# Optimization experiments

Hardware: AMD Instinct MI355X
Metric: run time of the kernel (lower is better)

Reference implementation:

```python
import jax, jax.numpy as jnp
import numpy as np

N_NODES = 100000
N_EDGES = 3200000
STATE_DIM = 128
ACTION_DIM = 8


def _w(key, shape, scale=0.05):
    return (jax.random.normal(key, shape, dtype=jnp.float32) * scale)


def setup_inputs() -> dict:
    key = jax.random.key(0)
    ks = jax.random.split(key, 24)
    x = jax.random.normal(ks[0], (N_NODES, STATE_DIM), dtype=jnp.float32)
    edge_index = jax.random.randint(ks[1], (2, N_EDGES), 0, N_NODES, dtype=jnp.int64)
    inp = {
        "x": x,
        "edge_index": edge_index,
        # GCN layers (weights stored [in, out] so forward is x @ W + b)
        "W1": _w(ks[2], (STATE_DIM, 128)), "b1": jnp.zeros((128,), jnp.float32),
        "W2": _w(ks[3], (128, 128)),       "b2": jnp.zeros((128,), jnp.float32),
        "W3": _w(ks[4], (128, 64)),        "b3": jnp.zeros((64,), jnp.float32),
        # actor MLP 64->128->64->ACTION_DIM + softmax
        "Wa1": _w(ks[5], (64, 128)),  "ba1": jnp.zeros((128,), jnp.float32),
        "Wa2": _w(ks[6], (128, 64)),  "ba2": jnp.zeros((64,), jnp.float32),
        "Wa3": _w(ks[7], (64, ACTION_DIM)), "ba3": jnp.zeros((ACTION_DIM,), jnp.float32),
        # critic MLP 64->128->64->1
        "Wc1": _w(ks[8], (64, 128)),  "bc1": jnp.zeros((128,), jnp.float32),
        "Wc2": _w(ks[9], (128, 64)),  "bc2": jnp.zeros((64,), jnp.float32),
        "Wc3": _w(ks[10], (64, 1)),   "bc3": jnp.zeros((1,), jnp.float32),
    }
    return inp


def _gcn_conv(x, W, b, src, dst, norm):
    # GCNConv: D^{-1/2} (A + I) D^{-1/2} X W + b  (self loops already in src/dst)
    h = x @ W                                   # [N, out]
    msg = h[src] * norm[:, None]                # gather + per-edge scale
    agg = jax.ops.segment_sum(msg, dst, num_segments=N_NODES)
    return agg + b


def reference(x, edge_index,
              W1, b1, W2, b2, W3, b3,
              Wa1, ba1, Wa2, ba2, Wa3, ba3,
              Wc1, bc1, Wc2, bc2, Wc3, bc3):
    loop = jnp.arange(N_NODES, dtype=edge_index.dtype)
    src = jnp.concatenate([edge_index[0], loop])
    dst = jnp.concatenate([edge_index[1], loop])
    deg = jax.ops.segment_sum(jnp.ones_like(dst, dtype=x.dtype), dst,
                              num_segments=N_NODES)
    dinv = jax.lax.rsqrt(deg)                   # deg >= 1 via self loops
    norm = dinv[src] * dinv[dst]                # [E+N]

    # forward_gnn (dropout is identity in eval mode)
    h = jax.nn.relu(_gcn_conv(x, W1, b1, src, dst, norm))
    h = jax.nn.relu(_gcn_conv(h, W2, b2, src, dst, norm))
    h = _gcn_conv(h, W3, b3, src, dst, norm)    # [N, 64]

    a = jax.nn.relu(h @ Wa1 + ba1)
    a = jax.nn.relu(a @ Wa2 + ba2)
    probs = jax.nn.softmax(a @ Wa3 + ba3, axis=-1)   # [N, ACTION_DIM]

    c = jax.nn.relu(h @ Wc1 + bc1)
    c = jax.nn.relu(c @ Wc2 + bc2)
    values = c @ Wc3 + bc3                      # [N, 1]

    return jnp.concatenate([probs, values], axis=-1)  # [N, ACTION_DIM+1]
```

## Files before the change

kernel.cpp:

```cpp
#include <hip/hip_runtime.h>
#include <hip/hip_bf16.h>
#include <math.h>


#define WS_ALIGN(x) (((x) + 255) & ~(size_t)255)

constexpr int RNG  = 64;
constexpr int NRG  = 1563;
constexpr int NB   = 1024;
constexpr int CHK  = 16;

constexpr float S_FP8     = 64.0f;
constexpr float S_FP8_INV = 1.0f / 64.0f;

using bf16x8 = __attribute__((ext_vector_type(8))) short;
using f32x4  = __attribute__((ext_vector_type(4))) float;
using f32x2  = __attribute__((ext_vector_type(2))) float;

__device__ __forceinline__ float b2f(unsigned short u) {
    return __uint_as_float(((unsigned int)u) << 16);
}
__device__ __forceinline__ unsigned short f2b(float f) {
    __hip_bfloat16 hb = __float2bfloat16(f);
    return *(unsigned short*)&hb;
}
__device__ __forceinline__ unsigned char f2fp8(float f) {
    return (unsigned char)(__builtin_amdgcn_cvt_pk_fp8_f32(f, f, 0, false) & 0xff);
}
__device__ __forceinline__ int pad8(int v) { return (v + 7) & ~7; }

__device__ __forceinline__ void acc8(uint2 u, f32x2& a01, f32x2& a23,
                                     f32x2& a45, f32x2& a67) {
    a01 += __builtin_amdgcn_cvt_pk_f32_fp8((int)u.x, false);
    a23 += __builtin_amdgcn_cvt_pk_f32_fp8((int)u.x, true);
    a45 += __builtin_amdgcn_cvt_pk_f32_fp8((int)u.y, false);
    a67 += __builtin_amdgcn_cvt_pk_f32_fp8((int)u.y, true);
}


__global__ __launch_bounds__(256) void bucket_count_k(
    const int* __restrict__ dst, int* __restrict__ bcnt, int E) {
    __shared__ int c64[RNG];
    int b = blockIdx.x, t = threadIdx.x;
    if (t < RNG) c64[t] = 0;
    __syncthreads();
    int ec = (E + NB - 1) / NB;
    int e0 = b * ec, e1 = min(E, e0 + ec);
    for (int e = e0 + t; e < e1; e += 256) {
        int d = __builtin_nontemporal_load(dst + e);
        atomicAdd(&c64[d / NRG], 1);
    }
    __syncthreads();
    if (t < RNG) bcnt[t * NB + b] = c64[t];
}

__global__ __launch_bounds__(256) void rsum_k(
    const int* __restrict__ bcnt, int* __restrict__ base, int* __restrict__ rtot) {
    __shared__ int s[256];
    int r = blockIdx.x, t = threadIdx.x;
    const int* row = bcnt + (size_t)r * NB;
    int v[4], loc = 0;
#pragma unroll
    for (int j = 0; j < 4; j++) { v[j] = row[t * 4 + j]; loc += v[j]; }
    s[t] = loc;
    __syncthreads();
    for (int d = 1; d < 256; d <<= 1) {
        int x = (t >= d) ? s[t - d] : 0;
        __syncthreads();
        s[t] += x;
        __syncthreads();
    }
    int run = s[t] - loc;
    int* bp = base + (size_t)r * NB + t * 4;
#pragma unroll
    for (int j = 0; j < 4; j++) { bp[j] = run; run += v[j]; }
    if (t == 255) rtot[r] = s[255];
}

__global__ void rstart_k(const int* __restrict__ rtot, int* __restrict__ bstart, int E) {
    if (threadIdx.x == 0) {
        int run = 0;
        for (int r = 0; r < RNG; r++) { bstart[r] = run; run += rtot[r]; }
        bstart[RNG] = run;
    }
}

__global__ __launch_bounds__(256) void bucket_scatter_k(
    const int* __restrict__ src, const int* __restrict__ dst,
    const int* __restrict__ base, const int* __restrict__ bstart,
    unsigned* __restrict__ bucket, int E) {
    __shared__ int cur[RNG];
    int b = blockIdx.x, t = threadIdx.x;
    if (t < RNG) cur[t] = bstart[t] + base[(size_t)t * NB + b];
    __syncthreads();
    int ec = (E + NB - 1) / NB;
    int e0 = b * ec, e1 = min(E, e0 + ec);
    for (int e = e0 + t; e < e1; e += 256) {
        int d = __builtin_nontemporal_load(dst + e);
        int sv = __builtin_nontemporal_load(src + e);
        int r = d / NRG;
        int pos = atomicAdd(&cur[r], 1);
        bucket[pos] = ((unsigned)(d - r * NRG) << 17) | (unsigned)sv;
    }
}

__global__ __launch_bounds__(256) void hist_bucket_k(
    const unsigned* __restrict__ bucket, const int* __restrict__ bstart,
    int* __restrict__ hist) {
    __shared__ int h[NRG];
    int b = blockIdx.x, r = b & 63, c2 = b >> 6, t = threadIdx.x;
    for (int i = t; i < NRG; i += 256) h[i] = 0;
    int s0 = bstart[r], s1 = bstart[r + 1];
    int ec = (s1 - s0 + CHK - 1) / CHK;
    int e0 = s0 + c2 * ec, e1 = min(s1, e0 + ec);
    __syncthreads();
    for (int e = e0 + t; e < e1; e += 256) {
        unsigned v = __builtin_nontemporal_load(bucket + e);
        atomicAdd(&h[v >> 17], 1);
    }
    __syncthreads();
    int* out = hist + ((size_t)r * CHK + c2) * NRG;
    for (int i = t; i < NRG; i += 256) out[i] = h[i];
}

__global__ void sum_hist_dinv_k(const int* __restrict__ hist, int* __restrict__ cnt,
                                float* __restrict__ dinv, int N) {
    int i = blockIdx.x * 256 + threadIdx.x;
    if (i >= N) return;
    int r = i / NRG, li = i - r * NRG;
    const int* hp = hist + ((size_t)r * CHK) * NRG + li;
    int s = 0;
#pragma unroll
    for (int c = 0; c < CHK; c++) s += hp[(size_t)c * NRG];
    cnt[i] = s;
    dinv[i] = rsqrtf((float)s + 1.0f);
}

__global__ void chunk_sum_k(const int* __restrict__ cnt, int* __restrict__ bsum, int n) {
    __shared__ int sd[256];
    int t = threadIdx.x;
    int i = blockIdx.x * 256 + t;
    sd[t] = (i < n) ? pad8(cnt[i]) : 0;
    __syncthreads();
    for (int d = 128; d > 0; d >>= 1) {
        if (t < d) sd[t] += sd[t + d];
        __syncthreads();
    }
    if (t == 0) bsum[blockIdx.x] = sd[0];
}

__global__ void scan_mid_k(const int* __restrict__ bsum, int* __restrict__ boff,
                           int nb, int* __restrict__ rowptr, int N) {
    __shared__ int s[512];
    int t = threadIdx.x;
    s[t] = (t < nb) ? bsum[t] : 0;
    __syncthreads();
    if (t == 0) {
        int run = 0;
        for (int i = 0; i < nb; i++) { int v = s[i]; s[i] = run; run += v; }
        rowptr[N] = run;
    }
    __syncthreads();
    if (t < nb) boff[t] = s[t];
}

__global__ void scan_off_pad_k(const int* __restrict__ cnt, const int* __restrict__ boff,
                               int* __restrict__ rowptr, int* __restrict__ hist,
                               int* __restrict__ col, int N) {
    __shared__ int s[256];
    int t = threadIdx.x;
    int i = blockIdx.x * 256 + t;
    int cv = (i < N) ? cnt[i] : 0;
    int v = pad8(cv);
    if (i >= N) v = 0;
    s[t] = v;
    __syncthreads();
    for (int d = 1; d < 256; d <<= 1) {
        int x = (t >= d) ? s[t - d] : 0;
        __syncthreads();
        s[t] += x;
        __syncthreads();
    }
    if (i < N) {
        int rp = s[t] - v + boff[blockIdx.x];
        rowptr[i] = rp;
        int r = i / NRG, li = i - r * NRG;
        int* hp = hist + ((size_t)r * CHK) * NRG + li;
        int run = rp;
#pragma unroll
        for (int c = 0; c < CHK; c++) {
            int hv = hp[(size_t)c * NRG];
            hp[(size_t)c * NRG] = run;
            run += hv;
        }
        for (int e = rp + cv; e < rp + v; e++) col[e] = N;
    }
}

__global__ __launch_bounds__(256) void fill2_k(
    const unsigned* __restrict__ bucket, const int* __restrict__ bstart,
    const int* __restrict__ hist, int* __restrict__ col) {
    __shared__ int cur[NRG];
    int b = blockIdx.x, r = b & 63, c2 = b >> 6, t = threadIdx.x;
    const int* hp = hist + ((size_t)r * CHK + c2) * NRG;
    for (int i = t; i < NRG; i += 256) cur[i] = hp[i];
    int s0 = bstart[r], s1 = bstart[r + 1];
    int ec = (s1 - s0 + CHK - 1) / CHK;
    int e0 = s0 + c2 * ec, e1 = min(s1, e0 + ec);
    __syncthreads();
    for (int e = e0 + t; e < e1; e += 256) {
        unsigned v = __builtin_nontemporal_load(bucket + e);
        int slot = atomicAdd(&cur[v >> 17], 1);
        col[slot] = (int)(v & 0x1FFFFu);
    }
}


__global__ __launch_bounds__(256) void prep_w_k(
    const float* __restrict__ W1, const float* __restrict__ W2,
    const float* __restrict__ W3, const float* __restrict__ Wa1,
    const float* __restrict__ Wc1, const float* __restrict__ Wa2,
    const float* __restrict__ Wc2, unsigned short* __restrict__ wt) {
    int i = blockIdx.x * 256 + threadIdx.x;
    const float* W; int off, K, OUT;
    if (i < 16384)      { W = W1;  off = 0;     K = 128; OUT = 128; }
    else if (i < 32768) { W = W2;  off = 16384; K = 128; OUT = 128; }
    else if (i < 40960) { W = W3;  off = 32768; K = 128; OUT = 64; }
    else if (i < 49152) { W = Wa1; off = 40960; K = 64;  OUT = 128; }
    else if (i < 57344) { W = Wc1; off = 49152; K = 64;  OUT = 128; }
    else if (i < 65536) { W = Wa2; off = 57344; K = 128; OUT = 64; }
    else                { W = Wc2; off = 65536; K = 128; OUT = 64; }
    int j = i - off, k = j / OUT, n = j - k * OUT;
    wt[off + n * K + k] = f2b(W[j]);
}


template <int K, int OUT, int EPI, bool AF32>
__global__ __launch_bounds__(256) void gemm2_k(
    const void* __restrict__ Xv, int ldx, const unsigned short* __restrict__ Wt,
    const float* __restrict__ sb, const float* __restrict__ w3b,
    const float* __restrict__ b3, void* __restrict__ Yv, int N, int NT) {
    constexpr int LDK = K + 8;
    __shared__ __align__(16) unsigned short Bs[OUT * LDK];
    __shared__ __align__(16) unsigned short As[64 * LDK];
    int t = threadIdx.x;

    for (int g = t; g < OUT * (K / 8); g += 256) {
        int r = g / (K / 8), q = g - r * (K / 8);
        *(uint4*)&Bs[r * LDK + q * 8] = *(const uint4*)(Wt + r * K + q * 8);
    }

    int wv = t >> 6, lane = t & 63;
    int lm = lane & 15, lq = lane >> 4;
    constexpr int CT = OUT / 16;

    for (int tile = blockIdx.x; tile < NT; tile += gridDim.x) {
        int rowBase = tile * 64;

        if constexpr (AF32) {
            const float* X = (const float*)Xv;
            for (int g = t; g < 64 * (K / 8); g += 256) {
                int r = g / (K / 8), q = g - r * (K / 8);
                int gr = rowBase + r;
                unsigned short us[8];
                if (gr < N) {
                    float4 v0 = *(const float4*)(X + (size_t)gr * ldx + q * 8);
                    float4 v1 = *(const float4*)(X + (size_t)gr * ldx + q * 8 + 4);
                    us[0] = f2b(v0.x); us[1] = f2b(v0.y); us[2] = f2b(v0.z); us[3] = f2b(v0.w);
                    us[4] = f2b(v1.x); us[5] = f2b(v1.y); us[6] = f2b(v1.z); us[7] = f2b(v1.w);
                } else {
#pragma unroll
                    for (int j = 0; j < 8; j++) us[j] = 0;
                }
                *(uint4*)&As[r * LDK + q * 8] = *(uint4*)us;
            }
        } else {
            const unsigned short* X = (const unsigned short*)Xv;
            for (int g = t; g < 64 * (K / 8); g += 256) {
                int r = g / (K / 8), q = g - r * (K / 8);
                int gr = rowBase + r;
                uint4 v = make_uint4(0, 0, 0, 0);
                if (gr < N) v = *(const uint4*)(X + (size_t)gr * ldx + q * 8);
                *(uint4*)&As[r * LDK + q * 8] = v;
            }
        }
        __syncthreads();

        f32x4 acc[CT];
#pragma unroll
        for (int c = 0; c < CT; c++) acc[c] = (f32x4){0.f, 0.f, 0.f, 0.f};

        const unsigned short* arow = &As[(wv * 16 + lm) * LDK + lq * 8];
#pragma unroll
        for (int kt = 0; kt < K / 32; kt++) {
            bf16x8 a = *(const bf16x8*)(arow + kt * 32);
#pragma unroll
            for (int c = 0; c < CT; c++) {
                bf16x8 b = *(const bf16x8*)&Bs[(c * 16 + lm) * LDK + kt * 32 + lq * 8];
                acc[c] = __builtin_amdgcn_mfma_f32_16x16x32_bf16(a, b, acc[c], 0, 0, 0);
            }
        }

        int r0 = rowBase + wv * 16 + lq * 4;
        if constexpr (EPI == 0) {
#pragma unroll
            for (int r = 0; r < 4; r++) {
                int gr = r0 + r;
                float scale = (gr < N) ? sb[gr] * S_FP8 : 0.f;
#pragma unroll
                for (int c = 0; c < CT; c++) {
                    int colg = c * 16 + lm;
                    ((unsigned char*)Yv)[(size_t)gr * OUT + colg] = f2fp8(acc[c][r] * scale);
                }
            }
        } else if constexpr (EPI == 1) {
#pragma unroll
            for (int r = 0; r < 4; r++) {
                int gr = r0 + r;
                if (gr < N) {
#pragma unroll
                    for (int c = 0; c < CT; c++) {
                        int colg = c * 16 + lm;
                        float bb = (colg < 128) ? sb[colg] : w3b[colg - 128];
                        float v = fmaxf(acc[c][r] + bb, 0.f);
                        ((unsigned short*)Yv)[(size_t)gr * OUT + colg] = f2b(v);
                    }
                }
            }
        } else if constexpr (EPI == 2) {
            float l[4][8];
#pragma unroll
            for (int r = 0; r < 4; r++)
#pragma unroll
                for (int a = 0; a < 8; a++) l[r][a] = 0.f;
#pragma unroll
            for (int c = 0; c < CT; c++) {
                int colg = c * 16 + lm;
#pragma unroll
                for (int r = 0; r < 4; r++) {
                    float v = fmaxf(acc[c][r] + sb[colg], 0.f);
#pragma unroll
                    for (int a = 0; a < 8; a++)
                        l[r][a] = fmaf(v, w3b[colg * 8 + a], l[r][a]);
                }
            }
#pragma unroll
            for (int w = 1; w < 16; w <<= 1)
#pragma unroll
                for (int r = 0; r < 4; r++)
#pragma unroll
                    for (int a = 0; a < 8; a++)
                        l[r][a] += __shfl_xor(l[r][a], w, 64);
            if (lm < 8) {
#pragma unroll
                for (int r = 0; r < 4; r++) {
                    int gr = r0 + r;
                    if (gr < N) {
                        float lg[8], m = -1e30f;
#pragma unroll
                        for (int a = 0; a < 8; a++) { lg[a] = l[r][a] + b3[a]; m = fmaxf(m, lg[a]); }
                        float sum = 0.f;
#pragma unroll
                        for (int a = 0; a < 8; a++) { lg[a] = expf(lg[a] - m); sum += lg[a]; }
                        ((float*)Yv)[(size_t)gr * 9 + lm] = lg[lm] / sum;
                    }
                }
            }
        } else {
            float lv[4] = {0.f, 0.f, 0.f, 0.f};
#pragma unroll
            for (int c = 0; c < CT; c++) {
                int colg = c * 16 + lm;
#pragma unroll
                for (int r = 0; r < 4; r++) {
                    float v = fmaxf(acc[c][r] + sb[colg], 0.f);
                    lv[r] = fmaf(v, w3b[colg], lv[r]);
                }
            }
#pragma unroll
            for (int w = 1; w < 16; w <<= 1)
#pragma unroll
                for (int r = 0; r < 4; r++) lv[r] += __shfl_xor(lv[r], w, 64);
            if (lm == 0) {
#pragma unroll
                for (int r = 0; r < 4; r++) {
                    int gr = r0 + r;
                    if (gr < N) ((float*)Yv)[(size_t)gr * 9 + 8] = lv[r] + b3[0];
                }
            }
        }
        __syncthreads();
    }
}


template <bool RELU>
__global__ __launch_bounds__(256) void agg128_k(
    const unsigned char* __restrict__ H,
    const int* __restrict__ rowptr, const int* __restrict__ col,
    const float* __restrict__ dinv, const float* __restrict__ bias,
    unsigned short* __restrict__ Y, int N, int Ecap) {
    int tid = threadIdx.x;
    int node = blockIdx.x * 4 + (tid >> 6);
    if (node >= N) return;
    int lane = tid & 63;
    int grp = lane >> 4;
    int li8 = (lane & 15) * 8;

    f32x2 a01 = {0.f, 0.f}, a23 = {0.f, 0.f}, a45 = {0.f, 0.f}, a67 = {0.f, 0.f};
    if (grp == 0) {
        uint2 u = *(const uint2*)(H + (size_t)node * 128 + li8);
        acc8(u, a01, a23, a45, a67);
    }

    int start = rowptr[node], end = rowptr[node + 1];
    for (int e0 = start; e0 < end; e0 += 64) {
        int cv = col[min(e0 + lane, Ecap - 1)];
        int quads = min(64, end - e0) >> 2;
        for (int q = 0; q < quads; q += 2) {
            int s0 = __shfl(cv, 4 * q + grp, 64);
            int s1 = __shfl(cv, 4 * q + 4 + grp, 64);
            uint2 u0 = *(const uint2*)(H + (size_t)s0 * 128 + li8);
            uint2 u1 = *(const uint2*)(H + (size_t)s1 * 128 + li8);
            acc8(u0, a01, a23, a45, a67);
            acc8(u1, a01, a23, a45, a67);
        }
    }

#pragma unroll
    for (int w = 16; w < 64; w <<= 1) {
        a01[0] += __shfl_xor(a01[0], w, 64); a01[1] += __shfl_xor(a01[1], w, 64);
        a23[0] += __shfl_xor(a23[0], w, 64); a23[1] += __shfl_xor(a23[1], w, 64);
        a45[0] += __shfl_xor(a45[0], w, 64); a45[1] += __shfl_xor(a45[1], w, 64);
        a67[0] += __shfl_xor(a67[0], w, 64); a67[1] += __shfl_xor(a67[1], w, 64);
    }

    if (grp == 0) {
        float dv = dinv[node] * S_FP8_INV;
        float4 b0 = *(const float4*)(bias + li8);
        float4 b1 = *(const float4*)(bias + li8 + 4);
        float o0 = a01[0] * dv + b0.x, o1 = a01[1] * dv + b0.y;
        float o2 = a23[0] * dv + b0.z, o3 = a23[1] * dv + b0.w;
        float o4 = a45[0] * dv + b1.x, o5 = a45[1] * dv + b1.y;
        float o6 = a67[0] * dv + b1.z, o7 = a67[1] * dv + b1.w;
        if (RELU) {
            o0 = fmaxf(o0, 0.f); o1 = fmaxf(o1, 0.f); o2 = fmaxf(o2, 0.f); o3 = fmaxf(o3, 0.f);
            o4 = fmaxf(o4, 0.f); o5 = fmaxf(o5, 0.f); o6 = fmaxf(o6, 0.f); o7 = fmaxf(o7, 0.f);
        }
        unsigned short us[8] = {f2b(o0), f2b(o1), f2b(o2), f2b(o3),
                                f2b(o4), f2b(o5), f2b(o6), f2b(o7)};
        *(uint4*)(Y + (size_t)node * 128 + li8) = *(uint4*)us;
    }
}

__global__ __launch_bounds__(256) void agg64_k(
    const unsigned char* __restrict__ H,
    const int* __restrict__ rowptr, const int* __restrict__ col,
    const float* __restrict__ dinv, const float* __restrict__ bias,
    unsigned short* __restrict__ Y, int N, int Ecap) {
    int tid = threadIdx.x;
    int node = blockIdx.x * 4 + (tid >> 6);
    if (node >= N) return;
    int lane = tid & 63;
    int grp = lane >> 3;
    int li8 = (lane & 7) * 8;

    f32x2 a01 = {0.f, 0.f}, a23 = {0.f, 0.f}, a45 = {0.f, 0.f}, a67 = {0.f, 0.f};
    if (grp == 0) {
        uint2 u = *(const uint2*)(H + (size_t)node * 64 + li8);
        acc8(u, a01, a23, a45, a67);
    }

    int start = rowptr[node], end = rowptr[node + 1];
    for (int e0 = start; e0 < end; e0 += 64) {
        int cv = col[min(e0 + lane, Ecap - 1)];
        int octs = min(64, end - e0) >> 3;
        int o = 0;
        for (; o + 2 <= octs; o += 2) {
            int s0 = __shfl(cv, 8 * o + grp, 64);
            int s1 = __shfl(cv, 8 * o + 8 + grp, 64);
            uint2 u0 = *(const uint2*)(H + (size_t)s0 * 64 + li8);
            uint2 u1 = *(const uint2*)(H + (size_t)s1 * 64 + li8);
            acc8(u0, a01, a23, a45, a67);
            acc8(u1, a01, a23, a45, a67);
        }
        if (o < octs) {
            int s0 = __shfl(cv, 8 * o + grp, 64);
            uint2 u0 = *(const uint2*)(H + (size_t)s0 * 64 + li8);
            acc8(u0, a01, a23, a45, a67);
        }
    }

#pragma unroll
    for (int w = 8; w < 64; w <<= 1) {
        a01[0] += __shfl_xor(a01[0], w, 64); a01[1] += __shfl_xor(a01[1], w, 64);
        a23[0] += __shfl_xor(a23[0], w, 64); a23[1] += __shfl_xor(a23[1], w, 64);
        a45[0] += __shfl_xor(a45[0], w, 64); a45[1] += __shfl_xor(a45[1], w, 64);
        a67[0] += __shfl_xor(a67[0], w, 64); a67[1] += __shfl_xor(a67[1], w, 64);
    }

    if (grp == 0) {
        float dv = dinv[node] * S_FP8_INV;
        float4 b0 = *(const float4*)(bias + li8);
        float4 b1 = *(const float4*)(bias + li8 + 4);
        unsigned short us[8] = {
            f2b(a01[0] * dv + b0.x), f2b(a01[1] * dv + b0.y),
            f2b(a23[0] * dv + b0.z), f2b(a23[1] * dv + b0.w),
            f2b(a45[0] * dv + b1.x), f2b(a45[1] * dv + b1.y),
            f2b(a67[0] * dv + b1.z), f2b(a67[1] * dv + b1.w)};
        *(uint4*)(Y + (size_t)node * 64 + li8) = *(uint4*)us;
    }
}


extern "C" void kernel_launch(void* const* d_in, const int* in_sizes, int n_in,
                              void* d_out, int out_size, void* d_ws, size_t ws_size,
                              hipStream_t stream) {
    const float* x   = (const float*)d_in[0];
    const int*   ei  = (const int*)d_in[1];
    const float* W1  = (const float*)d_in[2];  const float* b1  = (const float*)d_in[3];
    const float* W2  = (const float*)d_in[4];  const float* b2  = (const float*)d_in[5];
    const float* W3  = (const float*)d_in[6];  const float* b3  = (const float*)d_in[7];
    const float* Wa1 = (const float*)d_in[8];  const float* ba1 = (const float*)d_in[9];
    const float* Wa2 = (const float*)d_in[10]; const float* ba2 = (const float*)d_in[11];
    const float* Wa3 = (const float*)d_in[12]; const float* ba3 = (const float*)d_in[13];
    const float* Wc1 = (const float*)d_in[14]; const float* bc1 = (const float*)d_in[15];
    const float* Wc2 = (const float*)d_in[16]; const float* bc2 = (const float*)d_in[17];
    const float* Wc3 = (const float*)d_in[18]; const float* bc3 = (const float*)d_in[19];
    float* out = (float*)d_out;

    const int N = in_sizes[0] / 128;
    const int E = in_sizes[1] / 2;
    const int* src = ei;
    const int* dst = ei + E;
    const int Ecap = E + 8 * N;
    const int Npad = ((N + 63) / 64) * 64;
    const int NT   = (N + 63) / 64;

    size_t off = 0;
    auto take = [&](size_t bytes) { size_t o = off; off = WS_ALIGN(off + bytes); return o; };
    char* ws = (char*)d_ws;
    unsigned short* h3     = (unsigned short*)(ws + take((size_t)N * 64 * 2));
    unsigned short* h      = (unsigned short*)(ws + take((size_t)N * 128 * 2));
    unsigned char*  hpr8   = (unsigned char*) (ws + take((size_t)(Npad + 64) * 128));
    int*            col    = (int*)(ws + take((size_t)Ecap * 4));
    unsigned short* wt     = (unsigned short*)(ws + take(73728 * 2));
    float* dinv   = (float*)(ws + take((size_t)(N + 64) * 4));
    int*   cnt    = (int*)  (ws + take((size_t)N * 4));
    int*   rowptr = (int*)  (ws + take((size_t)(N + 1) * 4));
    int*   bcnt   = (int*)  (ws + take((size_t)RNG * NB * 4));
    int*   base   = (int*)  (ws + take((size_t)RNG * NB * 4));
    int*   rtot   = (int*)  (ws + take(RNG * 4));
    int*   bstart = (int*)  (ws + take((RNG + 1) * 4));
    int*   bsum   = (int*)  (ws + take(512 * 4));
    int*   boff   = (int*)  (ws + take(512 * 4));
    unsigned* bucket = (unsigned*)h;
    int* hist = (int*)h3;
    unsigned short* A1C1 = (unsigned short*)h;
    (void)ws_size; (void)n_in; (void)out_size;

    const int nb  = (N + 255) / 256;
    const int gN  = (N + 255) / 256;
    const int GG  = 512;

    prep_w_k<<<288, 256, 0, stream>>>(W1, W2, W3, Wa1, Wc1, Wa2, Wc2, wt);
    const unsigned short* W1t  = wt;
    const unsigned short* W2t  = wt + 16384;
    const unsigned short* W3t  = wt + 32768;
    const unsigned short* Wh1t = wt + 40960;
    const unsigned short* Wa2t = wt + 57344;
    const unsigned short* Wc2t = wt + 65536;

    bucket_count_k<<<NB, 256, 0, stream>>>(dst, bcnt, E);
    rsum_k<<<RNG, 256, 0, stream>>>(bcnt, base, rtot);
    rstart_k<<<1, 64, 0, stream>>>(rtot, bstart, E);
    bucket_scatter_k<<<NB, 256, 0, stream>>>(src, dst, base, bstart, bucket, E);
    hist_bucket_k<<<RNG * CHK, 256, 0, stream>>>(bucket, bstart, hist);
    sum_hist_dinv_k<<<gN, 256, 0, stream>>>(hist, cnt, dinv, N);
    chunk_sum_k<<<nb, 256, 0, stream>>>(cnt, bsum, N);
    scan_mid_k<<<1, 512, 0, stream>>>(bsum, boff, nb, rowptr, N);
    scan_off_pad_k<<<nb, 256, 0, stream>>>(cnt, boff, rowptr, hist, col, N);
    fill2_k<<<RNG * CHK, 256, 0, stream>>>(bucket, bstart, hist, col);

    gemm2_k<128, 128, 0, true><<<GG, 256, 0, stream>>>(
        x, 128, W1t, dinv, nullptr, nullptr, hpr8, N, NT);
    agg128_k<true><<<(N + 3) / 4, 256, 0, stream>>>(hpr8, rowptr, col, dinv, b1, h, N, Ecap);
    gemm2_k<128, 128, 0, false><<<GG, 256, 0, stream>>>(
        h, 128, W2t, dinv, nullptr, nullptr, hpr8, N, NT);
    agg128_k<true><<<(N + 3) / 4, 256, 0, stream>>>(hpr8, rowptr, col, dinv, b2, h, N, Ecap);
    gemm2_k<128, 64, 0, false><<<GG, 256, 0, stream>>>(
        h, 128, W3t, dinv, nullptr, nullptr, hpr8, N, NT);
    agg64_k<<<(N + 3) / 4, 256, 0, stream>>>(hpr8, rowptr, col, dinv, b3, h3, N, Ecap);

    gemm2_k<64, 256, 1, false><<<GG, 256, 0, stream>>>(
        h3, 64, Wh1t, ba1, bc1, nullptr, A1C1, N, NT);
    gemm2_k<128, 64, 2, false><<<GG, 256, 0, stream>>>(
        A1C1, 256, Wa2t, ba2, Wa3, ba3, out, N, NT);
    gemm2_k<128, 64, 3, false><<<GG, 256, 0, stream>>>(
        A1C1 + 128, 256, Wc2t, bc2, Wc3, bc3, out, N, NT);
}
```

Baseline: 502.2 us.

## Store intermediate activations in FP8 instead of BF16 between layers

Aggregation outputs and the actor/critic hidden layer are now written as scaled FP8 bytes instead of BF16. The GEMM A-loads decode them back to BF16 with a new input mode that undoes the scale. This halves the traffic for intermediates across all stages, at the cost of extra conversion ALU work and reduced accuracy. The degree-histogram sum and chunk-sum kernels are also fused into one launch, and workspace buffers are reorganized.

Result: no change. 507.1 us (+1.0%).

```diff
diff --git a/kernel.cpp b/kernel.cpp
--- a/kernel.cpp
+++ b/kernel.cpp
@@ -12,6 +12,8 @@
 
 constexpr float S_FP8     = 64.0f;
 constexpr float S_FP8_INV = 1.0f / 64.0f;
+constexpr float S2        = 32.0f;
+constexpr float S2I       = 1.0f / 32.0f;
 
 using bf16x8 = __attribute__((ext_vector_type(8))) short;
 using f32x4  = __attribute__((ext_vector_type(4))) float;
@@ -77,7 +79,7 @@
     if (t == 255) rtot[r] = s[255];
 }
 
-__global__ void rstart_k(const int* __restrict__ rtot, int* __restrict__ bstart, int E) {
+__global__ void rstart_k(const int* __restrict__ rtot, int* __restrict__ bstart) {
     if (threadIdx.x == 0) {
         int run = 0;
         for (int r = 0; r < RNG; r++) { bstart[r] = run; run += rtot[r]; }
@@ -123,24 +125,22 @@
     for (int i = t; i < NRG; i += 256) out[i] = h[i];
 }
 
-__global__ void sum_hist_dinv_k(const int* __restrict__ hist, int* __restrict__ cnt,
-                                float* __restrict__ dinv, int N) {
-    int i = blockIdx.x * 256 + threadIdx.x;
-    if (i >= N) return;
-    int r = i / NRG, li = i - r * NRG;
-    const int* hp = hist + ((size_t)r * CHK) * NRG + li;
-    int s = 0;
-#pragma unroll
-    for (int c = 0; c < CHK; c++) s += hp[(size_t)c * NRG];
-    cnt[i] = s;
-    dinv[i] = rsqrtf((float)s + 1.0f);
-}
-
-__global__ void chunk_sum_k(const int* __restrict__ cnt, int* __restrict__ bsum, int n) {
+__global__ void sum_hist_dinv_chunk_k(const int* __restrict__ hist,
+                                      int* __restrict__ cnt, float* __restrict__ dinv,
+                                      int* __restrict__ bsum, int N) {
     __shared__ int sd[256];
     int t = threadIdx.x;
     int i = blockIdx.x * 256 + t;
-    sd[t] = (i < n) ? pad8(cnt[i]) : 0;
+    int s = 0;
+    if (i < N) {
+        int r = i / NRG, li = i - r * NRG;
+        const int* hp = hist + ((size_t)r * CHK) * NRG + li;
+#pragma unroll
+        for (int c = 0; c < CHK; c++) s += hp[(size_t)c * NRG];
+        cnt[i] = s;
+        dinv[i] = rsqrtf((float)s + 1.0f);
+    }
+    sd[t] = (i < N) ? pad8(s) : 0;
     __syncthreads();
     for (int d = 128; d > 0; d >>= 1) {
         if (t < d) sd[t] += sd[t + d];
@@ -171,8 +171,7 @@
     int t = threadIdx.x;
     int i = blockIdx.x * 256 + t;
     int cv = (i < N) ? cnt[i] : 0;
-    int v = pad8(cv);
-    if (i >= N) v = 0;
+    int v = (i < N) ? pad8(cv) : 0;
     s[t] = v;
     __syncthreads();
     for (int d = 1; d < 256; d <<= 1) {
@@ -235,12 +234,13 @@
 }
 
 
-template <int K, int OUT, int EPI, bool AF32>
+template <int K, int OUT, int EPI, int AMODE>
 __global__ __launch_bounds__(256) void gemm2_k(
     const void* __restrict__ Xv, int ldx, const unsigned short* __restrict__ Wt,
     const float* __restrict__ sb, const float* __restrict__ w3b,
     const float* __restrict__ b3, void* __restrict__ Yv, int N, int NT) {
     constexpr int LDK = K + 8;
+    constexpr float AIN = (AMODE == 2) ? S2I : 1.0f;
     __shared__ __align__(16) unsigned short Bs[OUT * LDK];
     __shared__ __align__(16) unsigned short As[64 * LDK];
     int t = threadIdx.x;
@@ -257,7 +257,7 @@
     for (int tile = blockIdx.x; tile < NT; tile += gridDim.x) {
         int rowBase = tile * 64;
 
-        if constexpr (AF32) {
+        if constexpr (AMODE == 0) {
             const float* X = (const float*)Xv;
             for (int g = t; g < 64 * (K / 8); g += 256) {
                 int r = g / (K / 8), q = g - r * (K / 8);
@@ -275,13 +275,24 @@
                 *(uint4*)&As[r * LDK + q * 8] = *(uint4*)us;
             }
         } else {
-            const unsigned short* X = (const unsigned short*)Xv;
+            const unsigned char* X = (const unsigned char*)Xv;
             for (int g = t; g < 64 * (K / 8); g += 256) {
                 int r = g / (K / 8), q = g - r * (K / 8);
                 int gr = rowBase + r;
-                uint4 v = make_uint4(0, 0, 0, 0);
-                if (gr < N) v = *(const uint4*)(X + (size_t)gr * ldx + q * 8);
-                *(uint4*)&As[r * LDK + q * 8] = v;
+                unsigned short us[8];
+                if (gr < N) {
+                    uint2 u = *(const uint2*)(X + (size_t)gr * ldx + q * 8);
+                    f32x2 v0 = __builtin_amdgcn_cvt_pk_f32_fp8((int)u.x, false);
+                    f32x2 v1 = __builtin_amdgcn_cvt_pk_f32_fp8((int)u.x, true);
+                    f32x2 v2 = __builtin_amdgcn_cvt_pk_f32_fp8((int)u.y, false);
+                    f32x2 v3 = __builtin_amdgcn_cvt_pk_f32_fp8((int)u.y, true);
+                    us[0] = f2b(v0[0]); us[1] = f2b(v0[1]); us[2] = f2b(v1[0]); us[3] = f2b(v1[1]);
+                    us[4] = f2b(v2[0]); us[5] = f2b(v2[1]); us[6] = f2b(v3[0]); us[7] = f2b(v3[1]);
+                } else {
+#pragma unroll
+                    for (int j = 0; j < 8; j++) us[j] = 0;
+                }
+                *(uint4*)&As[r * LDK + q * 8] = *(uint4*)us;
             }
         }
         __syncthreads();
@@ -306,7 +317,7 @@
 #pragma unroll
             for (int r = 0; r < 4; r++) {
                 int gr = r0 + r;
-                float scale = (gr < N) ? sb[gr] * S_FP8 : 0.f;
+                float scale = (gr < N) ? sb[gr] * (S_FP8 * AIN) : 0.f;
 #pragma unroll
                 for (int c = 0; c < CT; c++) {
                     int colg = c * 16 + lm;
@@ -322,8 +333,8 @@
                     for (int c = 0; c < CT; c++) {
                         int colg = c * 16 + lm;
                         float bb = (colg < 128) ? sb[colg] : w3b[colg - 128];
-                        float v = fmaxf(acc[c][r] + bb, 0.f);
-                        ((unsigned short*)Yv)[(size_t)gr * OUT + colg] = f2b(v);
+                        float v = fmaxf(acc[c][r] * AIN + bb, 0.f);
+                        ((unsigned char*)Yv)[(size_t)gr * OUT + colg] = f2fp8(v * S2);
                     }
                 }
             }
@@ -338,7 +349,7 @@
                 int colg = c * 16 + lm;
 #pragma unroll
                 for (int r = 0; r < 4; r++) {
-                    float v = fmaxf(acc[c][r] + sb[colg], 0.f);
+                    float v = fmaxf(acc[c][r] * AIN + sb[colg], 0.f);
 #pragma unroll
                     for (int a = 0; a < 8; a++)
                         l[r][a] = fmaf(v, w3b[colg * 8 + a], l[r][a]);
@@ -373,7 +384,7 @@
                 int colg = c * 16 + lm;
 #pragma unroll
                 for (int r = 0; r < 4; r++) {
-                    float v = fmaxf(acc[c][r] + sb[colg], 0.f);
+                    float v = fmaxf(acc[c][r] * AIN + sb[colg], 0.f);
                     lv[r] = fmaf(v, w3b[colg], lv[r]);
                 }
             }
@@ -399,7 +410,7 @@
     const unsigned char* __restrict__ H,
     const int* __restrict__ rowptr, const int* __restrict__ col,
     const float* __restrict__ dinv, const float* __restrict__ bias,
-    unsigned short* __restrict__ Y, int N, int Ecap) {
+    unsigned char* __restrict__ Y, int N, int Ecap) {
     int tid = threadIdx.x;
     int node = blockIdx.x * 4 + (tid >> 6);
     if (node >= N) return;
@@ -447,9 +458,9 @@
             o0 = fmaxf(o0, 0.f); o1 = fmaxf(o1, 0.f); o2 = fmaxf(o2, 0.f); o3 = fmaxf(o3, 0.f);
             o4 = fmaxf(o4, 0.f); o5 = fmaxf(o5, 0.f); o6 = fmaxf(o6, 0.f); o7 = fmaxf(o7, 0.f);
         }
-        unsigned short us[8] = {f2b(o0), f2b(o1), f2b(o2), f2b(o3),
-                                f2b(o4), f2b(o5), f2b(o6), f2b(o7)};
-        *(uint4*)(Y + (size_t)node * 128 + li8) = *(uint4*)us;
+        unsigned char us[8] = {f2fp8(o0 * S2), f2fp8(o1 * S2), f2fp8(o2 * S2), f2fp8(o3 * S2),
+                               f2fp8(o4 * S2), f2fp8(o5 * S2), f2fp8(o6 * S2), f2fp8(o7 * S2)};
+        *(uint2*)(Y + (size_t)node * 128 + li8) = *(uint2*)us;
     }
 }
 
@@ -457,7 +468,7 @@
     const unsigned char* __restrict__ H,
     const int* __restrict__ rowptr, const int* __restrict__ col,
     const float* __restrict__ dinv, const float* __restrict__ bias,
-    unsigned short* __restrict__ Y, int N, int Ecap) {
+    unsigned char* __restrict__ Y, int N, int Ecap) {
     int tid = threadIdx.x;
     int node = blockIdx.x * 4 + (tid >> 6);
     if (node >= N) return;
@@ -503,12 +514,12 @@
         float dv = dinv[node] * S_FP8_INV;
         float4 b0 = *(const float4*)(bias + li8);
         float4 b1 = *(const float4*)(bias + li8 + 4);
-        unsigned short us[8] = {
-            f2b(a01[0] * dv + b0.x), f2b(a01[1] * dv + b0.y),
-            f2b(a23[0] * dv + b0.z), f2b(a23[1] * dv + b0.w),
-            f2b(a45[0] * dv + b1.x), f2b(a45[1] * dv + b1.y),
-            f2b(a67[0] * dv + b1.z), f2b(a67[1] * dv + b1.w)};
-        *(uint4*)(Y + (size_t)node * 64 + li8) = *(uint4*)us;
+        unsigned char us[8] = {
+            f2fp8((a01[0] * dv + b0.x) * S2), f2fp8((a01[1] * dv + b0.y) * S2),
+            f2fp8((a23[0] * dv + b0.z) * S2), f2fp8((a23[1] * dv + b0.w) * S2),
+            f2fp8((a45[0] * dv + b1.x) * S2), f2fp8((a45[1] * dv + b1.y) * S2),
+            f2fp8((a67[0] * dv + b1.z) * S2), f2fp8((a67[1] * dv + b1.w) * S2)};
+        *(uint2*)(Y + (size_t)node * 64 + li8) = *(uint2*)us;
     }
 }
 
@@ -540,11 +551,11 @@
     size_t off = 0;
     auto take = [&](size_t bytes) { size_t o = off; off = WS_ALIGN(off + bytes); return o; };
     char* ws = (char*)d_ws;
-    unsigned short* h3     = (unsigned short*)(ws + take((size_t)N * 64 * 2));
-    unsigned short* h      = (unsigned short*)(ws + take((size_t)N * 128 * 2));
-    unsigned char*  hpr8   = (unsigned char*) (ws + take((size_t)(Npad + 64) * 128));
-    int*            col    = (int*)(ws + take((size_t)Ecap * 4));
-    unsigned short* wt     = (unsigned short*)(ws + take(73728 * 2));
+    unsigned char* P1   = (unsigned char*)(ws + take((size_t)(Npad + 64) * 128));
+    unsigned char* H1   = (unsigned char*)(ws + take((size_t)(Npad + 64) * 128));
+    unsigned char* A1C1 = (unsigned char*)(ws + take((size_t)N * 256));
+    int*           col  = (int*)(ws + take((size_t)Ecap * 4));
+    unsigned short* wt  = (unsigned short*)(ws + take(73728 * 2));
     float* dinv   = (float*)(ws + take((size_t)(N + 64) * 4));
     int*   cnt    = (int*)  (ws + take((size_t)N * 4));
     int*   rowptr = (int*)  (ws + take((size_t)(N + 1) * 4));
@@ -554,13 +565,11 @@
     int*   bstart = (int*)  (ws + take((RNG + 1) * 4));
     int*   bsum   = (int*)  (ws + take(512 * 4));
     int*   boff   = (int*)  (ws + take(512 * 4));
-    unsigned* bucket = (unsigned*)h;
-    int* hist = (int*)h3;
-    unsigned short* A1C1 = (unsigned short*)h;
+    unsigned* bucket = (unsigned*)A1C1;
+    int* hist = (int*)(A1C1 + (size_t)E * 4);
     (void)ws_size; (void)n_in; (void)out_size;
 
     const int nb  = (N + 255) / 256;
-    const int gN  = (N + 255) / 256;
     const int GG  = 512;
 
     prep_w_k<<<288, 256, 0, stream>>>(W1, W2, W3, Wa1, Wc1, Wa2, Wc2, wt);
@@ -573,29 +582,28 @@
 
     bucket_count_k<<<NB, 256, 0, stream>>>(dst, bcnt, E);
     rsum_k<<<RNG, 256, 0, stream>>>(bcnt, base, rtot);
-    rstart_k<<<1, 64, 0, stream>>>(rtot, bstart, E);
+    rstart_k<<<1, 64, 0, stream>>>(rtot, bstart);
     bucket_scatter_k<<<NB, 256, 0, stream>>>(src, dst, base, bstart, bucket, E);
     hist_bucket_k<<<RNG * CHK, 256, 0, stream>>>(bucket, bstart, hist);
-    sum_hist_dinv_k<<<gN, 256, 0, stream>>>(hist, cnt, dinv, N);
-    chunk_sum_k<<<nb, 256, 0, stream>>>(cnt, bsum, N);
+    sum_hist_dinv_chunk_k<<<nb, 256, 0, stream>>>(hist, cnt, dinv, bsum, N);
     scan_mid_k<<<1, 512, 0, stream>>>(bsum, boff, nb, rowptr, N);
     scan_off_pad_k<<<nb, 256, 0, stream>>>(cnt, boff, rowptr, hist, col, N);
     fill2_k<<<RNG * CHK, 256, 0, stream>>>(bucket, bstart, hist, col);
 
-    gemm2_k<128, 128, 0, true><<<GG, 256, 0, stream>>>(
-        x, 128, W1t, dinv, nullptr, nullptr, hpr8, N, NT);
-    agg128_k<true><<<(N + 3) / 4, 256, 0, stream>>>(hpr8, rowptr, col, dinv, b1, h, N, Ecap);
-    gemm2_k<128, 128, 0, false><<<GG, 256, 0, stream>>>(
-        h, 128, W2t, dinv, nullptr, nullptr, hpr8, N, NT);
-    agg128_k<true><<<(N + 3) / 4, 256, 0, stream>>>(hpr8, rowptr, col, dinv, b2, h, N, Ecap);
-    gemm2_k<128, 64, 0, false><<<GG, 256, 0, stream>>>(
-        h, 128, W3t, dinv, nullptr, nullptr, hpr8, N, NT);
-    agg64_k<<<(N + 3) / 4, 256, 0, stream>>>(hpr8, rowptr, col, dinv, b3, h3, N, Ecap);
-
-    gemm2_k<64, 256, 1, false><<<GG, 256, 0, stream>>>(
-        h3, 64, Wh1t, ba1, bc1, nullptr, A1C1, N, NT);
-    gemm2_k<128, 64, 2, false><<<GG, 256, 0, stream>>>(
+    gemm2_k<128, 128, 0, 0><<<GG, 256, 0, stream>>>(
+        x, 128, W1t, dinv, nullptr, nullptr, P1, N, NT);
+    agg128_k<true><<<(N + 3) / 4, 256, 0, stream>>>(P1, rowptr, col, dinv, b1, H1, N, Ecap);
+    gemm2_k<128, 128, 0, 2><<<GG, 256, 0, stream>>>(
+        H1, 128, W2t, dinv, nullptr, nullptr, P1, N, NT);
+    agg128_k<true><<<(N + 3) / 4, 256, 0, stream>>>(P1, rowptr, col, dinv, b2, H1, N, Ecap);
+    gemm2_k<128, 64, 0, 2><<<GG, 256, 0, stream>>>(
+        H1, 128, W3t, dinv, nullptr, nullptr, P1, N, NT);
+    agg64_k<<<(N + 3) / 4, 256, 0, stream>>>(P1, rowptr, col, dinv, b3, H1, N, Ecap);
+
+    gemm2_k<64, 256, 1, 2><<<GG, 256, 0, stream>>>(
+        H1, 64, Wh1t, ba1, bc1, nullptr, A1C1, N, NT);
+    gemm2_k<128, 64, 2, 2><<<GG, 256, 0, stream>>>(
         A1C1, 256, Wa2t, ba2, Wa3, ba3, out, N, NT);
-    gemm2_k<128, 64, 3, false><<<GG, 256, 0, stream>>>(
+    gemm2_k<128, 64, 3, 2><<<GG, 256, 0, stream>>>(
         A1C1 + 128, 256, Wc2t, bc2, Wc3, bc3, out, N, NT);
 }
```
